# Kernel optimization log

Hardware: AMD Instinct MI355X
Metric: run time of the kernel (lower is better)

The kernel has to match this reference:

```python
import jax, jax.numpy as jnp
import numpy as np

N, D_IN, N_CTRS, D_OUT = 65536, 64, 1024, 256


def setup_inputs() -> dict:
    key = jax.random.key(0)
    k_x, k_c, k_v = jax.random.split(key, 3)
    x = jax.random.normal(k_x, (N, D_IN), dtype=jnp.float32)
    # learned params: centers (init_ctrs 'random' draws from data scale), values (normal), scales s=ones
    ctrs = jax.random.normal(k_c, (N_CTRS, D_IN), dtype=jnp.float32)
    values = jax.random.normal(k_v, (N_CTRS, D_OUT), dtype=jnp.float32) * 1e-2
    s = jnp.ones((D_IN,), dtype=jnp.float32)
    return {"x": x, "ctrs": ctrs, "values": values, "s": s}


def reference(x, ctrs, values, s):
    # dist_sq[n,k] = sum_d (x[n,d]-ctrs[k,d])^2 * s[d]
    # expanded to avoid the (N, n_ctrs, d_in) broadcast intermediate:
    x_sq = jnp.einsum('nd,d->n', x * x, s)            # (N,)
    c_sq = jnp.einsum('kd,d->k', ctrs * ctrs, s)      # (K,)
    cross = jnp.einsum('nd,kd->nk', x * s, ctrs)      # (N, K)
    dist_sq = x_sq[:, None] + c_sq[None, :] - 2.0 * cross
    assignments = jax.nn.softmax(-dist_sq, axis=1)    # (N, K)
    return assignments @ values                        # (N, d_out)
```

## Files before the change

kernel.cpp:

```cpp
#include <hip/hip_runtime.h>

typedef _Float16 half_t;
typedef half_t f16x8 __attribute__((ext_vector_type(8)));
typedef float f32x4 __attribute__((ext_vector_type(4)));

#define LOG2E 1.44269504088896340736f

#define NROWS 65536
#define DIN   64
#define NCTRS 1024
#define DOUT  256

#define CSWZ_OFF 0
#define CSWZ_BYTES (128 * 1024)
#define VSWZ_OFF (CSWZ_OFF + CSWZ_BYTES)
#define VSWZ_BYTES (512 * 1024)
#define CSQ_OFF  (VSWZ_OFF + VSWZ_BYTES)

#define VT_STRIDE 260
#define CT_STRIDE 68

__global__ __launch_bounds__(256) void precompute_kernel(
    const float* __restrict__ ctrs, const float* __restrict__ values,
    const float* __restrict__ s, char* __restrict__ ws) {
  half_t* Cswz = (half_t*)(ws + CSWZ_OFF);
  half_t* Vswz = (half_t*)(ws + VSWZ_OFF);
  float* csq2 = (float*)(ws + CSQ_OFF);

  __shared__ half_t Vt[32 * VT_STRIDE];
  __shared__ half_t Ct[32 * CT_STRIDE];

  const int c = blockIdx.x, tid = threadIdx.x;

  for (int i = tid; i < 32 * 256; i += 256) {
    int r = i >> 8, col = i & 255;
    Vt[r * VT_STRIDE + col] = (half_t)values[(c * 32 + r) * DOUT + col];
  }
  for (int i = tid; i < 32 * 64; i += 256) {
    int r = i >> 6, col = i & 63;
    Ct[r * CT_STRIDE + col] = (half_t)ctrs[(c * 32 + r) * DIN + col];
  }
  if (tid < 32) {
    int k = c * 32 + tid;
    float acc = 0.0f;
    for (int d = 0; d < DIN; ++d) {
      float cv = ctrs[k * DIN + d];
      acc = fmaf(cv * cv, s[d], acc);
    }
    csq2[k] = acc * LOG2E;
  }
  __syncthreads();

  const int w = tid >> 6, l = tid & 63, l4 = l >> 4, lm = l & 15;

  {
    int ct = w >> 1, kt = w & 1;
    f16x8 v;
#pragma unroll
    for (int j = 0; j < 8; ++j)
      v[j] = Ct[(ct * 16 + lm) * CT_STRIDE + kt * 32 + l4 * 8 + j];
    *(f16x8*)(Cswz + ((c * 4 + w) * 64 + l) * 8) = v;
  }
#pragma unroll
  for (int q = 0; q < 4; ++q) {
    int sl = w * 4 + q;
    f16x8 v;
#pragma unroll
    for (int j = 0; j < 8; ++j)
      v[j] = Vt[(l4 * 8 + j) * VT_STRIDE + sl * 16 + lm];
    *(f16x8*)(Vswz + ((c * 16 + sl) * 64 + l) * 8) = v;
  }
}

__global__ __launch_bounds__(256, 2) void attn_kernel(
    const float* __restrict__ x, const float* __restrict__ s,
    const char* __restrict__ ws, float* __restrict__ out) {
  const half_t* Cswz = (const half_t*)(ws + CSWZ_OFF);
  const half_t* Vswz = (const half_t*)(ws + VSWZ_OFF);
  const float* csq2 = (const float*)(ws + CSQ_OFF);
  const f16x8* cbase = (const f16x8*)Cswz;
  const f16x8* vbase = (const f16x8*)Vswz;

  __shared__ half_t Plds[4 * 32 * 40];

  const int tid = threadIdx.x;
  const int w = tid >> 6, l = tid & 63, l4 = l >> 4, lm = l & 15;
  const int rowbase = blockIdx.x * 128 + w * 32;

  f16x8 A[2][2];
#pragma unroll
  for (int rt = 0; rt < 2; ++rt) {
#pragma unroll
    for (int kt = 0; kt < 2; ++kt) {
      int din = kt * 32 + l4 * 8;
      const float* src = x + (rowbase + rt * 16 + lm) * DIN + din;
      f16x8 a;
#pragma unroll
      for (int j = 0; j < 8; ++j) a[j] = (half_t)(src[j] * s[din + j]);
      A[rt][kt] = a;
    }
  }

  f16x8 ones;
#pragma unroll
  for (int j = 0; j < 8; ++j) ones[j] = (lm == 0) ? (half_t)1.0f : (half_t)0.0f;

  float m[2][4];
#pragma unroll
  for (int rt = 0; rt < 2; ++rt)
#pragma unroll
    for (int j = 0; j < 4; ++j) m[rt][j] = -1e30f;

  f16x8 nb0 = cbase[0 * 64 + l], nb1 = cbase[1 * 64 + l];
  f16x8 nb2 = cbase[2 * 64 + l], nb3 = cbase[3 * 64 + l];
  float ncs0 = csq2[lm], ncs1 = csq2[16 + lm];

  for (int c = 0; c < 32; ++c) {
    f16x8 b0 = nb0, b1 = nb1, b2 = nb2, b3 = nb3;
    float cs0 = ncs0, cs1 = ncs1;
    int cn = (c < 31) ? c + 1 : 31;
    nb0 = cbase[(cn * 4 + 0) * 64 + l];
    nb1 = cbase[(cn * 4 + 1) * 64 + l];
    nb2 = cbase[(cn * 4 + 2) * 64 + l];
    nb3 = cbase[(cn * 4 + 3) * 64 + l];
    ncs0 = csq2[cn * 32 + lm];
    ncs1 = csq2[cn * 32 + 16 + lm];
#pragma unroll
    for (int rt = 0; rt < 2; ++rt) {
      f32x4 a0 = {0.f, 0.f, 0.f, 0.f}, a1 = {0.f, 0.f, 0.f, 0.f};
      a0 = __builtin_amdgcn_mfma_f32_16x16x32_f16(A[rt][0], b0, a0, 0, 0, 0);
      a0 = __builtin_amdgcn_mfma_f32_16x16x32_f16(A[rt][1], b1, a0, 0, 0, 0);
      a1 = __builtin_amdgcn_mfma_f32_16x16x32_f16(A[rt][0], b2, a1, 0, 0, 0);
      a1 = __builtin_amdgcn_mfma_f32_16x16x32_f16(A[rt][1], b3, a1, 0, 0, 0);
#pragma unroll
      for (int j = 0; j < 4; ++j) {
        float v0 = fmaf(a0[j], 2.0f * LOG2E, -cs0);
        float v1 = fmaf(a1[j], 2.0f * LOG2E, -cs1);
        m[rt][j] = fmaxf(m[rt][j], fmaxf(v0, v1));
      }
    }
  }
#pragma unroll
  for (int rt = 0; rt < 2; ++rt)
#pragma unroll
    for (int j = 0; j < 4; ++j) {
      float v = m[rt][j];
      v = fmaxf(v, __shfl_xor(v, 1));
      v = fmaxf(v, __shfl_xor(v, 2));
      v = fmaxf(v, __shfl_xor(v, 4));
      v = fmaxf(v, __shfl_xor(v, 8));
      m[rt][j] = v;
    }

  f32x4 O[2][16];
  f32x4 L[2];
#pragma unroll
  for (int rt = 0; rt < 2; ++rt) {
    L[rt] = (f32x4){0.f, 0.f, 0.f, 0.f};
#pragma unroll
    for (int u = 0; u < 16; ++u) O[rt][u] = (f32x4){0.f, 0.f, 0.f, 0.f};
  }

  half_t* pw = Plds + w * (32 * 40);

  for (int c = 0; c < 32; ++c) {
    f16x8 b0 = cbase[(c * 4 + 0) * 64 + l];
    f16x8 b1 = cbase[(c * 4 + 1) * 64 + l];
    f16x8 b2 = cbase[(c * 4 + 2) * 64 + l];
    f16x8 b3 = cbase[(c * 4 + 3) * 64 + l];
    float cs0 = csq2[c * 32 + lm], cs1 = csq2[c * 32 + 16 + lm];
    f16x8 pa[2];
#pragma unroll
    for (int rt = 0; rt < 2; ++rt) {
      f32x4 a0 = {0.f, 0.f, 0.f, 0.f}, a1 = {0.f, 0.f, 0.f, 0.f};
      a0 = __builtin_amdgcn_mfma_f32_16x16x32_f16(A[rt][0], b0, a0, 0, 0, 0);
      a0 = __builtin_amdgcn_mfma_f32_16x16x32_f16(A[rt][1], b1, a0, 0, 0, 0);
      a1 = __builtin_amdgcn_mfma_f32_16x16x32_f16(A[rt][0], b2, a1, 0, 0, 0);
      a1 = __builtin_amdgcn_mfma_f32_16x16x32_f16(A[rt][1], b3, a1, 0, 0, 0);
#pragma unroll
      for (int j = 0; j < 4; ++j) {
        float v0 = fmaf(a0[j], 2.0f * LOG2E, -cs0) - m[rt][j];
        float v1 = fmaf(a1[j], 2.0f * LOG2E, -cs1) - m[rt][j];
        float p0 = __builtin_amdgcn_exp2f(v0);
        float p1 = __builtin_amdgcn_exp2f(v1);
        int pr = (rt * 16 + l4 * 4 + j) * 40 + lm;
        pw[pr] = (half_t)p0;
        pw[pr + 16] = (half_t)p1;
      }
      pa[rt] = *(const f16x8*)(pw + (rt * 16 + lm) * 40 + l4 * 8);
    }
#pragma unroll
    for (int u = 0; u < 16; ++u) {
      f16x8 vb = vbase[(c * 16 + u) * 64 + l];
      O[0][u] = __builtin_amdgcn_mfma_f32_16x16x32_f16(pa[0], vb, O[0][u], 0, 0, 0);
      O[1][u] = __builtin_amdgcn_mfma_f32_16x16x32_f16(pa[1], vb, O[1][u], 0, 0, 0);
    }
    L[0] = __builtin_amdgcn_mfma_f32_16x16x32_f16(pa[0], ones, L[0], 0, 0, 0);
    L[1] = __builtin_amdgcn_mfma_f32_16x16x32_f16(pa[1], ones, L[1], 0, 0, 0);
  }

#pragma unroll
  for (int rt = 0; rt < 2; ++rt) {
#pragma unroll
    for (int j = 0; j < 4; ++j) {
      float lv = __shfl(L[rt][j], l & 48);
      float inv = 1.0f / fmaxf(lv, 1e-30f);
      int row = rowbase + rt * 16 + l4 * 4 + j;
      float* po = out + row * DOUT + lm;
#pragma unroll
      for (int ct = 0; ct < 16; ++ct) po[ct * 16] = O[rt][ct][j] * inv;
    }
  }
}

extern "C" void kernel_launch(void* const* d_in, const int* in_sizes, int n_in,
                              void* d_out, int out_size, void* d_ws, size_t ws_size,
                              hipStream_t stream) {
  const float* x = (const float*)d_in[0];
  const float* ctrs = (const float*)d_in[1];
  const float* values = (const float*)d_in[2];
  const float* s = (const float*)d_in[3];
  float* out = (float*)d_out;
  char* ws = (char*)d_ws;

  hipLaunchKernelGGL(precompute_kernel, dim3(32), dim3(256), 0, stream,
                     ctrs, values, s, ws);
  hipLaunchKernelGGL(attn_kernel, dim3(512), dim3(256), 0, stream,
                     x, s, ws, out);
}
```

Measured before the change: 142.1 us.

## Switch to single-pass online softmax with lazy rescale and LDS-staged values

Removes the separate max pass over all centers and instead keeps a running max per row, rescaling the accumulators only when the new block max exceeds the current one by a threshold. The matmuls are transposed so that probabilities stay in registers, using permlane swaps in place of an LDS round-trip. Value tiles are double-buffered into LDS with direct global-to-LDS loads so they overlap compute. The precompute kernel is vectorised with float4 loads. Skipping the first pass roughly halves the distance MFMAs and the center loads. The cost is a wave-wide branch for rescaling and exp values that may reach up to 2^8 in fp16.

New measurement: 142.4 us. No clear change (+0.2%).

```diff
diff --git a/kernel.cpp b/kernel.cpp
--- a/kernel.cpp
+++ b/kernel.cpp
@@ -3,6 +3,7 @@
 typedef _Float16 half_t;
 typedef half_t f16x8 __attribute__((ext_vector_type(8)));
 typedef float f32x4 __attribute__((ext_vector_type(4)));
+typedef unsigned int u32x2 __attribute__((ext_vector_type(2)));
 
 #define LOG2E 1.44269504088896340736f
 
@@ -19,6 +20,13 @@
 
 #define VT_STRIDE 260
 #define CT_STRIDE 68
+
+#define RESCALE_THR 8.0f
+
+#define GLOAD_LDS16(g, l)                                                      \
+  __builtin_amdgcn_global_load_lds(                                            \
+      (const __attribute__((address_space(1))) void*)(const void*)(g),         \
+      (__attribute__((address_space(3))) void*)(void*)(l), 16, 0, 0)
 
 __global__ __launch_bounds__(256) void precompute_kernel(
     const float* __restrict__ ctrs, const float* __restrict__ values,
@@ -32,22 +40,36 @@
 
   const int c = blockIdx.x, tid = threadIdx.x;
 
-  for (int i = tid; i < 32 * 256; i += 256) {
-    int r = i >> 8, col = i & 255;
-    Vt[r * VT_STRIDE + col] = (half_t)values[(c * 32 + r) * DOUT + col];
-  }
-  for (int i = tid; i < 32 * 64; i += 256) {
-    int r = i >> 6, col = i & 63;
-    Ct[r * CT_STRIDE + col] = (half_t)ctrs[(c * 32 + r) * DIN + col];
-  }
-  if (tid < 32) {
-    int k = c * 32 + tid;
+#pragma unroll
+  for (int i = 0; i < 8; ++i) {
+    int idx = i * 256 + tid;
+    int r = idx >> 6, c4 = (idx & 63) * 4;
+    float4 v = ((const float4*)values)[(size_t)(c * 32 + r) * 64 + (idx & 63)];
+    Vt[r * VT_STRIDE + c4 + 0] = (half_t)v.x;
+    Vt[r * VT_STRIDE + c4 + 1] = (half_t)v.y;
+    Vt[r * VT_STRIDE + c4 + 2] = (half_t)v.z;
+    Vt[r * VT_STRIDE + c4 + 3] = (half_t)v.w;
+  }
+#pragma unroll
+  for (int i = 0; i < 2; ++i) {
+    int idx = i * 256 + tid;
+    int r = idx >> 4, c4 = (idx & 15) * 4;
+    float4 v = ((const float4*)ctrs)[(size_t)(c * 32 + r) * 16 + (idx & 15)];
+    Ct[r * CT_STRIDE + c4 + 0] = (half_t)v.x;
+    Ct[r * CT_STRIDE + c4 + 1] = (half_t)v.y;
+    Ct[r * CT_STRIDE + c4 + 2] = (half_t)v.z;
+    Ct[r * CT_STRIDE + c4 + 3] = (half_t)v.w;
+  }
+  {
+    int k = tid >> 3, dg = (tid & 7) * 8;
+    const float* cp = ctrs + (size_t)(c * 32 + k) * DIN + dg;
     float acc = 0.0f;
-    for (int d = 0; d < DIN; ++d) {
-      float cv = ctrs[k * DIN + d];
-      acc = fmaf(cv * cv, s[d], acc);
-    }
-    csq2[k] = acc * LOG2E;
+#pragma unroll
+    for (int j = 0; j < 8; ++j) acc = fmaf(cp[j] * cp[j], s[dg + j], acc);
+    acc += __shfl_xor(acc, 1);
+    acc += __shfl_xor(acc, 2);
+    acc += __shfl_xor(acc, 4);
+    if ((tid & 7) == 0) csq2[c * 32 + k] = acc * LOG2E;
   }
   __syncthreads();
 
@@ -75,17 +97,20 @@
 __global__ __launch_bounds__(256, 2) void attn_kernel(
     const float* __restrict__ x, const float* __restrict__ s,
     const char* __restrict__ ws, float* __restrict__ out) {
-  const half_t* Cswz = (const half_t*)(ws + CSWZ_OFF);
-  const half_t* Vswz = (const half_t*)(ws + VSWZ_OFF);
+  const f16x8* cbase = (const f16x8*)(ws + CSWZ_OFF);
+  const char* Vraw = ws + VSWZ_OFF;
   const float* csq2 = (const float*)(ws + CSQ_OFF);
-  const f16x8* cbase = (const f16x8*)Cswz;
-  const f16x8* vbase = (const f16x8*)Vswz;
-
-  __shared__ half_t Plds[4 * 32 * 40];
+
+  __shared__ __attribute__((aligned(16))) char vbuf[2][16384];
 
   const int tid = threadIdx.x;
   const int w = tid >> 6, l = tid & 63, l4 = l >> 4, lm = l & 15;
   const int rowbase = blockIdx.x * 128 + w * 32;
+
+#pragma unroll
+  for (int i = 0; i < 4; ++i) {
+    GLOAD_LDS16(Vraw + i * 4096 + tid * 16, &vbuf[0][i * 4096 + w * 1024]);
+  }
 
   f16x8 A[2][2];
 #pragma unroll
@@ -105,110 +130,108 @@
 #pragma unroll
   for (int j = 0; j < 8; ++j) ones[j] = (lm == 0) ? (half_t)1.0f : (half_t)0.0f;
 
-  float m[2][4];
-#pragma unroll
-  for (int rt = 0; rt < 2; ++rt)
-#pragma unroll
-    for (int j = 0; j < 4; ++j) m[rt][j] = -1e30f;
-
-  f16x8 nb0 = cbase[0 * 64 + l], nb1 = cbase[1 * 64 + l];
-  f16x8 nb2 = cbase[2 * 64 + l], nb3 = cbase[3 * 64 + l];
-  float ncs0 = csq2[lm], ncs1 = csq2[16 + lm];
-
+  f32x4 O[2][16];
+  f32x4 Lacc[2];
+  float m[2] = {-1e30f, -1e30f};
+#pragma unroll
+  for (int rt = 0; rt < 2; ++rt) {
+    Lacc[rt] = (f32x4){0.f, 0.f, 0.f, 0.f};
+#pragma unroll
+    for (int u = 0; u < 16; ++u) O[rt][u] = (f32x4){0.f, 0.f, 0.f, 0.f};
+  }
+
+#pragma unroll 1
   for (int c = 0; c < 32; ++c) {
-    f16x8 b0 = nb0, b1 = nb1, b2 = nb2, b3 = nb3;
-    float cs0 = ncs0, cs1 = ncs1;
-    int cn = (c < 31) ? c + 1 : 31;
-    nb0 = cbase[(cn * 4 + 0) * 64 + l];
-    nb1 = cbase[(cn * 4 + 1) * 64 + l];
-    nb2 = cbase[(cn * 4 + 2) * 64 + l];
-    nb3 = cbase[(cn * 4 + 3) * 64 + l];
-    ncs0 = csq2[cn * 32 + lm];
-    ncs1 = csq2[cn * 32 + 16 + lm];
-#pragma unroll
-    for (int rt = 0; rt < 2; ++rt) {
-      f32x4 a0 = {0.f, 0.f, 0.f, 0.f}, a1 = {0.f, 0.f, 0.f, 0.f};
-      a0 = __builtin_amdgcn_mfma_f32_16x16x32_f16(A[rt][0], b0, a0, 0, 0, 0);
-      a0 = __builtin_amdgcn_mfma_f32_16x16x32_f16(A[rt][1], b1, a0, 0, 0, 0);
-      a1 = __builtin_amdgcn_mfma_f32_16x16x32_f16(A[rt][0], b2, a1, 0, 0, 0);
-      a1 = __builtin_amdgcn_mfma_f32_16x16x32_f16(A[rt][1], b3, a1, 0, 0, 0);
-#pragma unroll
-      for (int j = 0; j < 4; ++j) {
-        float v0 = fmaf(a0[j], 2.0f * LOG2E, -cs0);
-        float v1 = fmaf(a1[j], 2.0f * LOG2E, -cs1);
-        m[rt][j] = fmaxf(m[rt][j], fmaxf(v0, v1));
-      }
-    }
-  }
-#pragma unroll
-  for (int rt = 0; rt < 2; ++rt)
-#pragma unroll
-    for (int j = 0; j < 4; ++j) {
-      float v = m[rt][j];
-      v = fmaxf(v, __shfl_xor(v, 1));
-      v = fmaxf(v, __shfl_xor(v, 2));
-      v = fmaxf(v, __shfl_xor(v, 4));
-      v = fmaxf(v, __shfl_xor(v, 8));
-      m[rt][j] = v;
-    }
-
-  f32x4 O[2][16];
-  f32x4 L[2];
-#pragma unroll
-  for (int rt = 0; rt < 2; ++rt) {
-    L[rt] = (f32x4){0.f, 0.f, 0.f, 0.f};
-#pragma unroll
-    for (int u = 0; u < 16; ++u) O[rt][u] = (f32x4){0.f, 0.f, 0.f, 0.f};
-  }
-
-  half_t* pw = Plds + w * (32 * 40);
-
-  for (int c = 0; c < 32; ++c) {
+    const int cur = c & 1;
+    asm volatile("s_waitcnt vmcnt(0)" ::: "memory");
+    __builtin_amdgcn_s_barrier();
+    __builtin_amdgcn_sched_barrier(0);
+
     f16x8 b0 = cbase[(c * 4 + 0) * 64 + l];
     f16x8 b1 = cbase[(c * 4 + 1) * 64 + l];
     f16x8 b2 = cbase[(c * 4 + 2) * 64 + l];
     f16x8 b3 = cbase[(c * 4 + 3) * 64 + l];
-    float cs0 = csq2[c * 32 + lm], cs1 = csq2[c * 32 + 16 + lm];
-    f16x8 pa[2];
+    f32x4 cs0 = *(const f32x4*)(csq2 + c * 32 + l4 * 4);
+    f32x4 cs1 = *(const f32x4*)(csq2 + c * 32 + 16 + l4 * 4);
+    __builtin_amdgcn_sched_barrier(0);
+
+    if (c < 31) {
+      const char* src = Vraw + (size_t)(c + 1) * 16384;
+#pragma unroll
+      for (int i = 0; i < 4; ++i) {
+        GLOAD_LDS16(src + i * 4096 + tid * 16,
+                    &vbuf[cur ^ 1][i * 4096 + w * 1024]);
+      }
+    }
+    __builtin_amdgcn_sched_barrier(0);
+
+    f16x8 pb[2];
 #pragma unroll
     for (int rt = 0; rt < 2; ++rt) {
-      f32x4 a0 = {0.f, 0.f, 0.f, 0.f}, a1 = {0.f, 0.f, 0.f, 0.f};
-      a0 = __builtin_amdgcn_mfma_f32_16x16x32_f16(A[rt][0], b0, a0, 0, 0, 0);
-      a0 = __builtin_amdgcn_mfma_f32_16x16x32_f16(A[rt][1], b1, a0, 0, 0, 0);
-      a1 = __builtin_amdgcn_mfma_f32_16x16x32_f16(A[rt][0], b2, a1, 0, 0, 0);
-      a1 = __builtin_amdgcn_mfma_f32_16x16x32_f16(A[rt][1], b3, a1, 0, 0, 0);
+      f32x4 t0 = {0.f, 0.f, 0.f, 0.f}, t1 = {0.f, 0.f, 0.f, 0.f};
+      t0 = __builtin_amdgcn_mfma_f32_16x16x32_f16(b0, A[rt][0], t0, 0, 0, 0);
+      t0 = __builtin_amdgcn_mfma_f32_16x16x32_f16(b1, A[rt][1], t0, 0, 0, 0);
+      t1 = __builtin_amdgcn_mfma_f32_16x16x32_f16(b2, A[rt][0], t1, 0, 0, 0);
+      t1 = __builtin_amdgcn_mfma_f32_16x16x32_f16(b3, A[rt][1], t1, 0, 0, 0);
+
+      float v0[4], v1[4];
+      float pm = -1e30f;
 #pragma unroll
       for (int j = 0; j < 4; ++j) {
-        float v0 = fmaf(a0[j], 2.0f * LOG2E, -cs0) - m[rt][j];
-        float v1 = fmaf(a1[j], 2.0f * LOG2E, -cs1) - m[rt][j];
-        float p0 = __builtin_amdgcn_exp2f(v0);
-        float p1 = __builtin_amdgcn_exp2f(v1);
-        int pr = (rt * 16 + l4 * 4 + j) * 40 + lm;
-        pw[pr] = (half_t)p0;
-        pw[pr + 16] = (half_t)p1;
-      }
-      pa[rt] = *(const f16x8*)(pw + (rt * 16 + lm) * 40 + l4 * 8);
-    }
+        v0[j] = fmaf(t0[j], 2.0f * LOG2E, -cs0[j]);
+        v1[j] = fmaf(t1[j], 2.0f * LOG2E, -cs1[j]);
+        pm = fmaxf(pm, fmaxf(v0[j], v1[j]));
+      }
+      pm = fmaxf(pm, __shfl_xor(pm, 16));
+      pm = fmaxf(pm, __shfl_xor(pm, 32));
+
+      if (__any(pm > m[rt] + RESCALE_THR)) {
+        float mn = fmaxf(m[rt], pm);
+        float f = __builtin_amdgcn_exp2f(m[rt] - mn);
+        m[rt] = mn;
+        Lacc[rt] *= f;
+#pragma unroll
+        for (int u = 0; u < 16; ++u) O[rt][u] *= f;
+      }
+
+      unsigned wds[4];
+#pragma unroll
+      for (int h = 0; h < 2; ++h) {
+        union { half_t h2[2]; unsigned u; } qa, qb;
+        qa.h2[0] = (half_t)__builtin_amdgcn_exp2f(v0[2 * h] - m[rt]);
+        qa.h2[1] = (half_t)__builtin_amdgcn_exp2f(v0[2 * h + 1] - m[rt]);
+        qb.h2[0] = (half_t)__builtin_amdgcn_exp2f(v1[2 * h] - m[rt]);
+        qb.h2[1] = (half_t)__builtin_amdgcn_exp2f(v1[2 * h + 1] - m[rt]);
+        u32x2 sw1 = __builtin_amdgcn_permlane32_swap(qa.u, qb.u, false, false);
+        u32x2 sw2 = __builtin_amdgcn_permlane16_swap(sw1.x, sw1.y, false, false);
+        wds[h] = sw2.x;
+        wds[h + 2] = sw2.y;
+      }
+      union { unsigned u[4]; f16x8 v; } pk;
+      pk.u[0] = wds[0]; pk.u[1] = wds[1]; pk.u[2] = wds[2]; pk.u[3] = wds[3];
+      pb[rt] = pk.v;
+    }
+
+    const char* vb = &vbuf[cur][l * 16];
 #pragma unroll
     for (int u = 0; u < 16; ++u) {
-      f16x8 vb = vbase[(c * 16 + u) * 64 + l];
-      O[0][u] = __builtin_amdgcn_mfma_f32_16x16x32_f16(pa[0], vb, O[0][u], 0, 0, 0);
-      O[1][u] = __builtin_amdgcn_mfma_f32_16x16x32_f16(pa[1], vb, O[1][u], 0, 0, 0);
-    }
-    L[0] = __builtin_amdgcn_mfma_f32_16x16x32_f16(pa[0], ones, L[0], 0, 0, 0);
-    L[1] = __builtin_amdgcn_mfma_f32_16x16x32_f16(pa[1], ones, L[1], 0, 0, 0);
+      f16x8 vf = *(const f16x8*)(vb + u * 1024);
+      O[0][u] = __builtin_amdgcn_mfma_f32_16x16x32_f16(vf, pb[0], O[0][u], 0, 0, 0);
+      O[1][u] = __builtin_amdgcn_mfma_f32_16x16x32_f16(vf, pb[1], O[1][u], 0, 0, 0);
+    }
+    Lacc[0] = __builtin_amdgcn_mfma_f32_16x16x32_f16(ones, pb[0], Lacc[0], 0, 0, 0);
+    Lacc[1] = __builtin_amdgcn_mfma_f32_16x16x32_f16(ones, pb[1], Lacc[1], 0, 0, 0);
   }
 
 #pragma unroll
   for (int rt = 0; rt < 2; ++rt) {
-#pragma unroll
-    for (int j = 0; j < 4; ++j) {
-      float lv = __shfl(L[rt][j], l & 48);
-      float inv = 1.0f / fmaxf(lv, 1e-30f);
-      int row = rowbase + rt * 16 + l4 * 4 + j;
-      float* po = out + row * DOUT + lm;
-#pragma unroll
-      for (int ct = 0; ct < 16; ++ct) po[ct * 16] = O[rt][ct][j] * inv;
+    float lv = __shfl(Lacc[rt][0], lm);
+    float inv = 1.0f / fmaxf(lv, 1e-30f);
+    float* po = out + (size_t)(rowbase + rt * 16 + lm) * DOUT + l4 * 4;
+#pragma unroll
+    for (int u = 0; u < 16; ++u) {
+      f32x4 ov = O[rt][u] * inv;
+      *(f32x4*)(po + u * 16) = ov;
     }
   }
 }
```

## Split precompute across more blocks and prefetch centers in softmax pass

Applied to the files above, without the earlier changes.

The precompute kernel now launches 256 blocks instead of 32. Each block converts and swizzles a 32-column slice of values using float4 loads, and the center conversion and norm computation are spread over more threads with a shuffle reduction. The second pass of the attention kernel now prefetches the next chunk's center fragments one iteration ahead, as the first pass already did. The aim is to shorten the serial precompute stage and hide global-load latency in the main loop, at the cost of a few extra registers.

Measured after the change: 234.8 us. +65.2%, slower.

```diff
diff --git a/kernel.cpp b/kernel.cpp
--- a/kernel.cpp
+++ b/kernel.cpp
@@ -17,7 +17,6 @@
 #define VSWZ_BYTES (512 * 1024)
 #define CSQ_OFF  (VSWZ_OFF + VSWZ_BYTES)
 
-#define VT_STRIDE 260
 #define CT_STRIDE 68
 
 __global__ __launch_bounds__(256) void precompute_kernel(
@@ -27,48 +26,59 @@
   half_t* Vswz = (half_t*)(ws + VSWZ_OFF);
   float* csq2 = (float*)(ws + CSQ_OFF);
 
-  __shared__ half_t Vt[32 * VT_STRIDE];
+  __shared__ half_t Vt[32 * 36];
   __shared__ half_t Ct[32 * CT_STRIDE];
 
-  const int c = blockIdx.x, tid = threadIdx.x;
-
-  for (int i = tid; i < 32 * 256; i += 256) {
-    int r = i >> 8, col = i & 255;
-    Vt[r * VT_STRIDE + col] = (half_t)values[(c * 32 + r) * DOUT + col];
-  }
-  for (int i = tid; i < 32 * 64; i += 256) {
-    int r = i >> 6, col = i & 63;
-    Ct[r * CT_STRIDE + col] = (half_t)ctrs[(c * 32 + r) * DIN + col];
-  }
-  if (tid < 32) {
-    int k = c * 32 + tid;
-    float acc = 0.0f;
-    for (int d = 0; d < DIN; ++d) {
-      float cv = ctrs[k * DIN + d];
-      acc = fmaf(cv * cv, s[d], acc);
-    }
-    csq2[k] = acc * LOG2E;
+  const int bid = blockIdx.x, tid = threadIdx.x;
+  const int c = bid & 31, part = bid >> 5;
+  const int w = tid >> 6, l = tid & 63, l4 = l >> 4, lm = l & 15;
+
+  {
+    int r = tid >> 3, f4 = tid & 7;
+    float4 v = ((const float4*)values)[(size_t)(c * 32 + r) * 64 + part * 8 + f4];
+    half_t* d = Vt + r * 36 + f4 * 4;
+    d[0] = (half_t)v.x; d[1] = (half_t)v.y;
+    d[2] = (half_t)v.z; d[3] = (half_t)v.w;
+  }
+  if (part == 0) {
+#pragma unroll
+    for (int i = 0; i < 2; ++i) {
+      int idx = i * 256 + tid;
+      int r = idx >> 4, c4 = (idx & 15) * 4;
+      float4 v = ((const float4*)ctrs)[(size_t)(c * 32 + r) * 16 + (idx & 15)];
+      Ct[r * CT_STRIDE + c4 + 0] = (half_t)v.x;
+      Ct[r * CT_STRIDE + c4 + 1] = (half_t)v.y;
+      Ct[r * CT_STRIDE + c4 + 2] = (half_t)v.z;
+      Ct[r * CT_STRIDE + c4 + 3] = (half_t)v.w;
+    }
+    {
+      int k = tid >> 3, dg = (tid & 7) * 8;
+      const float* cp = ctrs + (size_t)(c * 32 + k) * DIN + dg;
+      float acc = 0.0f;
+#pragma unroll
+      for (int j = 0; j < 8; ++j) acc = fmaf(cp[j] * cp[j], s[dg + j], acc);
+      acc += __shfl_xor(acc, 1);
+      acc += __shfl_xor(acc, 2);
+      acc += __shfl_xor(acc, 4);
+      if ((tid & 7) == 0) csq2[c * 32 + k] = acc * LOG2E;
+    }
   }
   __syncthreads();
 
-  const int w = tid >> 6, l = tid & 63, l4 = l >> 4, lm = l & 15;
-
-  {
+  if (w < 2) {
+    int sl = part * 2 + w;
+    f16x8 v;
+#pragma unroll
+    for (int j = 0; j < 8; ++j) v[j] = Vt[(l4 * 8 + j) * 36 + w * 16 + lm];
+    *(f16x8*)(Vswz + ((c * 16 + sl) * 64 + l) * 8) = v;
+  }
+  if (part == 0) {
     int ct = w >> 1, kt = w & 1;
     f16x8 v;
 #pragma unroll
     for (int j = 0; j < 8; ++j)
       v[j] = Ct[(ct * 16 + lm) * CT_STRIDE + kt * 32 + l4 * 8 + j];
     *(f16x8*)(Cswz + ((c * 4 + w) * 64 + l) * 8) = v;
-  }
-#pragma unroll
-  for (int q = 0; q < 4; ++q) {
-    int sl = w * 4 + q;
-    f16x8 v;
-#pragma unroll
-    for (int j = 0; j < 8; ++j)
-      v[j] = Vt[(l4 * 8 + j) * VT_STRIDE + sl * 16 + lm];
-    *(f16x8*)(Vswz + ((c * 16 + sl) * 64 + l) * 8) = v;
   }
 }
 
@@ -111,32 +121,34 @@
 #pragma unroll
     for (int j = 0; j < 4; ++j) m[rt][j] = -1e30f;
 
-  f16x8 nb0 = cbase[0 * 64 + l], nb1 = cbase[1 * 64 + l];
-  f16x8 nb2 = cbase[2 * 64 + l], nb3 = cbase[3 * 64 + l];
-  float ncs0 = csq2[lm], ncs1 = csq2[16 + lm];
-
-  for (int c = 0; c < 32; ++c) {
-    f16x8 b0 = nb0, b1 = nb1, b2 = nb2, b3 = nb3;
-    float cs0 = ncs0, cs1 = ncs1;
-    int cn = (c < 31) ? c + 1 : 31;
-    nb0 = cbase[(cn * 4 + 0) * 64 + l];
-    nb1 = cbase[(cn * 4 + 1) * 64 + l];
-    nb2 = cbase[(cn * 4 + 2) * 64 + l];
-    nb3 = cbase[(cn * 4 + 3) * 64 + l];
-    ncs0 = csq2[cn * 32 + lm];
-    ncs1 = csq2[cn * 32 + 16 + lm];
-#pragma unroll
-    for (int rt = 0; rt < 2; ++rt) {
-      f32x4 a0 = {0.f, 0.f, 0.f, 0.f}, a1 = {0.f, 0.f, 0.f, 0.f};
-      a0 = __builtin_amdgcn_mfma_f32_16x16x32_f16(A[rt][0], b0, a0, 0, 0, 0);
-      a0 = __builtin_amdgcn_mfma_f32_16x16x32_f16(A[rt][1], b1, a0, 0, 0, 0);
-      a1 = __builtin_amdgcn_mfma_f32_16x16x32_f16(A[rt][0], b2, a1, 0, 0, 0);
-      a1 = __builtin_amdgcn_mfma_f32_16x16x32_f16(A[rt][1], b3, a1, 0, 0, 0);
-#pragma unroll
-      for (int j = 0; j < 4; ++j) {
-        float v0 = fmaf(a0[j], 2.0f * LOG2E, -cs0);
-        float v1 = fmaf(a1[j], 2.0f * LOG2E, -cs1);
-        m[rt][j] = fmaxf(m[rt][j], fmaxf(v0, v1));
+  {
+    f16x8 nb0 = cbase[0 * 64 + l], nb1 = cbase[1 * 64 + l];
+    f16x8 nb2 = cbase[2 * 64 + l], nb3 = cbase[3 * 64 + l];
+    float ncs0 = csq2[lm], ncs1 = csq2[16 + lm];
+
+    for (int c = 0; c < 32; ++c) {
+      f16x8 b0 = nb0, b1 = nb1, b2 = nb2, b3 = nb3;
+      float cs0 = ncs0, cs1 = ncs1;
+      int cn = (c < 31) ? c + 1 : 31;
+      nb0 = cbase[(cn * 4 + 0) * 64 + l];
+      nb1 = cbase[(cn * 4 + 1) * 64 + l];
+      nb2 = cbase[(cn * 4 + 2) * 64 + l];
+      nb3 = cbase[(cn * 4 + 3) * 64 + l];
+      ncs0 = csq2[cn * 32 + lm];
+      ncs1 = csq2[cn * 32 + 16 + lm];
+#pragma unroll
+      for (int rt = 0; rt < 2; ++rt) {
+        f32x4 a0 = {0.f, 0.f, 0.f, 0.f}, a1 = {0.f, 0.f, 0.f, 0.f};
+        a0 = __builtin_amdgcn_mfma_f32_16x16x32_f16(A[rt][0], b0, a0, 0, 0, 0);
+        a0 = __builtin_amdgcn_mfma_f32_16x16x32_f16(A[rt][1], b1, a0, 0, 0, 0);
+        a1 = __builtin_amdgcn_mfma_f32_16x16x32_f16(A[rt][0], b2, a1, 0, 0, 0);
+        a1 = __builtin_amdgcn_mfma_f32_16x16x32_f16(A[rt][1], b3, a1, 0, 0, 0);
+#pragma unroll
+        for (int j = 0; j < 4; ++j) {
+          float v0 = fmaf(a0[j], 2.0f * LOG2E, -cs0);
+          float v1 = fmaf(a1[j], 2.0f * LOG2E, -cs1);
+          m[rt][j] = fmaxf(m[rt][j], fmaxf(v0, v1));
+        }
       }
     }
   }
@@ -163,40 +175,47 @@
 
   half_t* pw = Plds + w * (32 * 40);
 
-  for (int c = 0; c < 32; ++c) {
-    f16x8 b0 = cbase[(c * 4 + 0) * 64 + l];
-    f16x8 b1 = cbase[(c * 4 + 1) * 64 + l];
-    f16x8 b2 = cbase[(c * 4 + 2) * 64 + l];
-    f16x8 b3 = cbase[(c * 4 + 3) * 64 + l];
-    float cs0 = csq2[c * 32 + lm], cs1 = csq2[c * 32 + 16 + lm];
-    f16x8 pa[2];
-#pragma unroll
-    for (int rt = 0; rt < 2; ++rt) {
-      f32x4 a0 = {0.f, 0.f, 0.f, 0.f}, a1 = {0.f, 0.f, 0.f, 0.f};
-      a0 = __builtin_amdgcn_mfma_f32_16x16x32_f16(A[rt][0], b0, a0, 0, 0, 0);
-      a0 = __builtin_amdgcn_mfma_f32_16x16x32_f16(A[rt][1], b1, a0, 0, 0, 0);
-      a1 = __builtin_amdgcn_mfma_f32_16x16x32_f16(A[rt][0], b2, a1, 0, 0, 0);
-      a1 = __builtin_amdgcn_mfma_f32_16x16x32_f16(A[rt][1], b3, a1, 0, 0, 0);
-#pragma unroll
-      for (int j = 0; j < 4; ++j) {
-        float v0 = fmaf(a0[j], 2.0f * LOG2E, -cs0) - m[rt][j];
-        float v1 = fmaf(a1[j], 2.0f * LOG2E, -cs1) - m[rt][j];
-        float p0 = __builtin_amdgcn_exp2f(v0);
-        float p1 = __builtin_amdgcn_exp2f(v1);
-        int pr = (rt * 16 + l4 * 4 + j) * 40 + lm;
-        pw[pr] = (half_t)p0;
-        pw[pr + 16] = (half_t)p1;
+  {
+    f16x8 nb0 = cbase[0 * 64 + l], nb1 = cbase[1 * 64 + l];
+    f16x8 nb2 = cbase[2 * 64 + l], nb3 = cbase[3 * 64 + l];
+
+    for (int c = 0; c < 32; ++c) {
+      f16x8 b0 = nb0, b1 = nb1, b2 = nb2, b3 = nb3;
+      int cn = (c < 31) ? c + 1 : 31;
+      nb0 = cbase[(cn * 4 + 0) * 64 + l];
+      nb1 = cbase[(cn * 4 + 1) * 64 + l];
+      nb2 = cbase[(cn * 4 + 2) * 64 + l];
+      nb3 = cbase[(cn * 4 + 3) * 64 + l];
+      float cs0 = csq2[c * 32 + lm], cs1 = csq2[c * 32 + 16 + lm];
+      f16x8 pa[2];
+#pragma unroll
+      for (int rt = 0; rt < 2; ++rt) {
+        f32x4 a0 = {0.f, 0.f, 0.f, 0.f}, a1 = {0.f, 0.f, 0.f, 0.f};
+        a0 = __builtin_amdgcn_mfma_f32_16x16x32_f16(A[rt][0], b0, a0, 0, 0, 0);
+        a0 = __builtin_amdgcn_mfma_f32_16x16x32_f16(A[rt][1], b1, a0, 0, 0, 0);
+        a1 = __builtin_amdgcn_mfma_f32_16x16x32_f16(A[rt][0], b2, a1, 0, 0, 0);
+        a1 = __builtin_amdgcn_mfma_f32_16x16x32_f16(A[rt][1], b3, a1, 0, 0, 0);
+#pragma unroll
+        for (int j = 0; j < 4; ++j) {
+          float v0 = fmaf(a0[j], 2.0f * LOG2E, -cs0) - m[rt][j];
+          float v1 = fmaf(a1[j], 2.0f * LOG2E, -cs1) - m[rt][j];
+          float p0 = __builtin_amdgcn_exp2f(v0);
+          float p1 = __builtin_amdgcn_exp2f(v1);
+          int pr = (rt * 16 + l4 * 4 + j) * 40 + lm;
+          pw[pr] = (half_t)p0;
+          pw[pr + 16] = (half_t)p1;
+        }
+        pa[rt] = *(const f16x8*)(pw + (rt * 16 + lm) * 40 + l4 * 8);
       }
-      pa[rt] = *(const f16x8*)(pw + (rt * 16 + lm) * 40 + l4 * 8);
-    }
-#pragma unroll
-    for (int u = 0; u < 16; ++u) {
-      f16x8 vb = vbase[(c * 16 + u) * 64 + l];
-      O[0][u] = __builtin_amdgcn_mfma_f32_16x16x32_f16(pa[0], vb, O[0][u], 0, 0, 0);
-      O[1][u] = __builtin_amdgcn_mfma_f32_16x16x32_f16(pa[1], vb, O[1][u], 0, 0, 0);
-    }
-    L[0] = __builtin_amdgcn_mfma_f32_16x16x32_f16(pa[0], ones, L[0], 0, 0, 0);
-    L[1] = __builtin_amdgcn_mfma_f32_16x16x32_f16(pa[1], ones, L[1], 0, 0, 0);
+#pragma unroll
+      for (int u = 0; u < 16; ++u) {
+        f16x8 vb = vbase[(c * 16 + u) * 64 + l];
+        O[0][u] = __builtin_amdgcn_mfma_f32_16x16x32_f16(pa[0], vb, O[0][u], 0, 0, 0);
+        O[1][u] = __builtin_amdgcn_mfma_f32_16x16x32_f16(pa[1], vb, O[1][u], 0, 0, 0);
+      }
+      L[0] = __builtin_amdgcn_mfma_f32_16x16x32_f16(pa[0], ones, L[0], 0, 0, 0);
+      L[1] = __builtin_amdgcn_mfma_f32_16x16x32_f16(pa[1], ones, L[1], 0, 0, 0);
+    }
   }
 
 #pragma unroll
@@ -223,7 +242,7 @@
   float* out = (float*)d_out;
   char* ws = (char*)d_ws;
 
-  hipLaunchKernelGGL(precompute_kernel, dim3(32), dim3(256), 0, stream,
+  hipLaunchKernelGGL(precompute_kernel, dim3(256), dim3(256), 0, stream,
                      ctrs, values, s, ws);
   hipLaunchKernelGGL(attn_kernel, dim3(512), dim3(256), 0, stream,
                      x, s, ws, out);
```
